# Performance work log

Hardware: AMD Instinct MI355X
Metric: run time of the kernel (lower is better)

## Reference

```python
import jax, jax.numpy as jnp
import numpy as np

K = 3          # kernel size
STRIDE = 1
PAD = 1
GROUPS = 32    # GroupNorm groups
EPS = 1e-5


def setup_inputs() -> dict:
    key = jax.random.key(0)
    ks = jax.random.split(key, 6)
    B, Cin, H, W, Cout = 4, 256, 64, 64, 256
    K2 = K * K
    x = jax.random.normal(ks[0], (B, Cin, H, W), jnp.float32)
    offset = jax.random.normal(ks[1], (B, 2 * K2, H, W), jnp.float32)
    mask = jax.random.uniform(ks[2], (B, K2, H, W), jnp.float32)
    weight = jax.random.normal(ks[3], (Cout, Cin, K, K), jnp.float32) * (1.0 / np.sqrt(Cin * K2))
    bias = jnp.zeros((Cout,), jnp.float32)
    gamma = jnp.ones((Cout,), jnp.float32)   # constant_init(norm, 1)
    beta = jnp.zeros((Cout,), jnp.float32)   # bias=0
    return {"x": x, "offset": offset, "mask": mask, "weight": weight,
            "bias": bias, "gamma": gamma, "beta": beta}


def _modulated_deform_conv(x, offset, mask, weight, bias):
    """DCNv2: bilinear-sample x at learned offsets, modulate by mask, conv-accumulate."""
    B, Cin, H, W = x.shape
    Cout = weight.shape[0]
    K2 = K * K
    Ho = (H + 2 * PAD - K) // STRIDE + 1
    Wo = (W + 2 * PAD - K) // STRIDE + 1

    # base sampling grid per kernel point: [K2, Ho, Wo]
    ky, kx = jnp.meshgrid(jnp.arange(K), jnp.arange(K), indexing='ij')
    ky = ky.reshape(K2).astype(jnp.float32)
    kx = kx.reshape(K2).astype(jnp.float32)
    hs = (jnp.arange(Ho) * STRIDE - PAD).astype(jnp.float32)
    ws = (jnp.arange(Wo) * STRIDE - PAD).astype(jnp.float32)

    off = offset.reshape(B, K2, 2, Ho, Wo)  # interleaved (dy, dx) per kernel point
    y = ky[None, :, None, None] + hs[None, None, :, None] + off[:, :, 0]   # [B,K2,Ho,Wo]
    xc = kx[None, :, None, None] + ws[None, None, None, :] + off[:, :, 1]  # [B,K2,Ho,Wo]

    y0 = jnp.floor(y)
    x0 = jnp.floor(xc)
    dy = y - y0
    dx = xc - x0
    y0i = y0.astype(jnp.int32)
    x0i = x0.astype(jnp.int32)

    x_flat = x.reshape(B, Cin, H * W)

    def corner(yi, xi, w):
        # corner-wise zero padding outside the image (matches mmcv bilinear)
        valid = (yi >= 0) & (yi <= H - 1) & (xi >= 0) & (xi <= W - 1)
        idx = jnp.clip(yi, 0, H - 1) * W + jnp.clip(xi, 0, W - 1)  # [B,K2,Ho,Wo]
        idx_f = idx.reshape(B, -1)
        v = jax.vmap(lambda xf, i: xf[:, i])(x_flat, idx_f)  # [B, Cin, K2*Ho*Wo]
        wv = (w * valid.astype(w.dtype)).reshape(B, 1, -1)
        return v * wv

    val = (corner(y0i,     x0i,     (1 - dy) * (1 - dx))
         + corner(y0i,     x0i + 1, (1 - dy) * dx)
         + corner(y0i + 1, x0i,     dy * (1 - dx))
         + corner(y0i + 1, x0i + 1, dy * dx))
    val = val.reshape(B, Cin, K2, Ho, Wo) * mask[:, None]  # modulate

    w_r = weight.reshape(Cout, Cin, K2)
    out = jnp.einsum('bckhw,ock->bohw', val, w_r) + bias[None, :, None, None]
    return out


def _group_norm(x, gamma, beta):
    B, C, H, W = x.shape
    g = x.reshape(B, GROUPS, C // GROUPS, H, W)
    mu = g.mean(axis=(2, 3, 4), keepdims=True)
    var = ((g - mu) ** 2).mean(axis=(2, 3, 4), keepdims=True)
    g = (g - mu) * jax.lax.rsqrt(var + EPS)
    return g.reshape(B, C, H, W) * gamma[None, :, None, None] + beta[None, :, None, None]


def reference(x, offset, mask, weight, bias, gamma, beta):
    out = _modulated_deform_conv(x, offset, mask, weight, bias)
    out = _group_norm(out, gamma, beta)
    return jax.nn.relu(out)
```

## Files before the change

### kernel.cpp

```cpp
#include <hip/hip_runtime.h>
#include <math.h>

#define BB    4
#define CIN   256
#define HH    64
#define WWID  64
#define COUT  256
#define KKS   3
#define K2    9
#define PADV  1
#define HWSZ  4096
#define GROUPS 32
#define CPG   8
#define EPSV  1e-5f
#define ROWB  4608
#define NKC   36

typedef __attribute__((ext_vector_type(8))) short bf16x8;
typedef __attribute__((ext_vector_type(4))) float f32x4;

#define GLOAD_LDS16(g, l) \
    __builtin_amdgcn_global_load_lds((const __attribute__((address_space(1))) unsigned int*)(g), \
                                     (__attribute__((address_space(3))) unsigned int*)(l), 16, 0, 0)

__device__ __forceinline__ unsigned short f2bf(float f) {
    unsigned u = __float_as_uint(f);
    u = (u + 0x7fffu + ((u >> 16) & 1u)) >> 16;
    return (unsigned short)u;
}
__device__ __forceinline__ float bflo(unsigned q) { return __uint_as_float(q << 16); }
__device__ __forceinline__ float bfhi(unsigned q) { return __uint_as_float(q & 0xffff0000u); }
__device__ __forceinline__ void fma8(float* f, float w, uint4 q) {
    f[0] += w * bflo(q.x); f[1] += w * bfhi(q.x);
    f[2] += w * bflo(q.y); f[3] += w * bfhi(q.y);
    f[4] += w * bflo(q.z); f[5] += w * bfhi(q.z);
    f[6] += w * bflo(q.w); f[7] += w * bfhi(q.w);
}

__global__ __launch_bounds__(256)
void k_pre(const float* __restrict__ x, unsigned short* __restrict__ xh,
           const float* __restrict__ w, unsigned short* __restrict__ wtb,
           float* __restrict__ gstat) {
    int t = threadIdx.x;
    if (blockIdx.x < 128) {
        __shared__ float tile[32][33];
        int hw0 = blockIdx.x * 32;
        int c0  = blockIdx.y * 32;
        int b   = blockIdx.z;
        int tx = t & 31, ty = t >> 5;
        const float* xp = x + (size_t)b * CIN * HWSZ;
        #pragma unroll
        for (int i = 0; i < 4; i++)
            tile[ty + i * 8][tx] = xp[(c0 + ty + i * 8) * HWSZ + hw0 + tx];
        __syncthreads();
        int j = t >> 3, cq = t & 7;
        union { unsigned short s[4]; uint2 d; } pk;
        #pragma unroll
        for (int k = 0; k < 4; k++) pk.s[k] = f2bf(tile[cq * 4 + k][j]);
        *(uint2*)((char*)xh + ((size_t)b * HWSZ * CIN + (size_t)(hw0 + j) * CIN + c0 + cq * 4) * 2) = pk.d;
    } else {
        if (blockIdx.y == 0 && blockIdx.z == 0)
            for (int i = t; i < BB * GROUPS * 2 + 8; i += 256) gstat[i] = 0.f;
        int idx = (blockIdx.y * 4 + blockIdx.z) * 256 + t;
        int co = idx >> 5, c8 = idx & 31;
        int cin0 = c8 * 8;
        int q = c8 >> 3, c = c8 & 7;
        int pc = c ^ (co & 7);
        for (int k2 = 0; k2 < K2; k2++) {
            union { unsigned short s[8]; uint4 qq; } pk;
            #pragma unroll
            for (int j = 0; j < 8; j++)
                pk.s[j] = f2bf(w[(co * CIN + cin0 + j) * K2 + k2]);
            int phys = co * ROWB + k2 * 512 + q * 128 + pc * 16;
            *(uint4*)((char*)wtb + phys) = pk.qq;
        }
    }
}

__global__ __launch_bounds__(256)
void k_conv(const unsigned short* __restrict__ wtb, const unsigned short* __restrict__ xh,
            const float* __restrict__ offset, const float* __restrict__ mask,
            const float* __restrict__ bias, float* __restrict__ out,
            float* __restrict__ gstat) {
    __shared__ unsigned short As[128 * 64];
    __shared__ unsigned short Bs[64 * 64];
    __shared__ int   cidx[64 * K2 * 4];
    __shared__ float cwgt[64 * K2 * 4];
    __shared__ float gs[16], gss[16];

    int lid = blockIdx.x;
    int j8  = lid >> 3;
    int mt  = j8 & 1;
    int strip = (lid & 7) * 32 + (j8 >> 1);
    int b = strip >> 6;
    int hwbase = (strip & 63) * 64;
    int m0 = mt * 128;

    int t = threadIdx.x, w = t >> 6, l = t & 63;
    int r16 = l & 15, half = l >> 4;
    int wm = w & 1, wn = w >> 1;
    int skey = r16 & 7;

    if (t < 16) { gs[t] = 0.f; gss[t] = 0.f; }

    for (int i = t; i < 64 * K2; i += 256) {
        int px = i / K2, k2 = i - px * K2;
        int hw = hwbase + px;
        int ho = hw >> 6, wo = hw & 63;
        int ky = k2 / KKS, kx = k2 - ky * KKS;
        float dy = offset[((b * (2 * K2) + k2 * 2 + 0) * HWSZ) + hw];
        float dx = offset[((b * (2 * K2) + k2 * 2 + 1) * HWSZ) + hw];
        float m  = mask[(b * K2 + k2) * HWSZ + hw];
        float y  = (float)(ky + ho - PADV) + dy;
        float xc = (float)(kx + wo - PADV) + dx;
        float y0f = floorf(y), x0f = floorf(xc);
        float fy = y - y0f, fx = xc - x0f;
        int y0 = (int)y0f, x0 = (int)x0f;
        int   yy[2] = { y0, y0 + 1 };
        int   xx[2] = { x0, x0 + 1 };
        float wy[2] = { 1.f - fy, fy };
        float wx[2] = { 1.f - fx, fx };
        #pragma unroll
        for (int ii = 0; ii < 2; ii++)
            #pragma unroll
            for (int jj = 0; jj < 2; jj++) {
                int yi = yy[ii], xi = xx[jj];
                bool valid = (yi >= 0) && (yi < HH) && (xi >= 0) && (xi < WWID);
                int yc  = min(max(yi, 0), HH - 1);
                int xcc = min(max(xi, 0), WWID - 1);
                cidx[i * 4 + ii * 2 + jj] = yc * WWID + xcc;
                cwgt[i * 4 + ii * 2 + jj] = valid ? (wy[ii] * wx[jj] * m) : 0.f;
            }
    }

    const char* ag[4]; unsigned short* lA[4];
    #pragma unroll
    for (int i = 0; i < 4; i++) {
        int o = i * 256 + t;
        ag[i] = (const char*)wtb + (size_t)(m0 + (o >> 3)) * ROWB + (o & 7) * 16;
        lA[i] = (unsigned short*)As + o * 8;
    }

    int sc  = t & 7;
    int px0 = t >> 3;
    const char* xb = (const char*)xh + (size_t)b * HWSZ * CIN * 2;
    int bofs0 = px0 * 64 + (sc ^ (px0 & 7)) * 8;
    int px1 = px0 + 32;
    int bofs1 = px1 * 64 + (sc ^ (px1 & 7)) * 8;

    f32x4 acc[4][2];
    #pragma unroll
    for (int mi = 0; mi < 4; mi++)
        #pragma unroll
        for (int ni = 0; ni < 2; ni++) acc[mi][ni] = (f32x4)0.f;

    __syncthreads();

    uint4 g[2][4]; float gw[2][4];
    #pragma unroll
    for (int it = 0; it < 2; it++) {
        int cb = ((it ? px1 : px0) * K2) * 4;
        #pragma unroll
        for (int c = 0; c < 4; c++) {
            gw[it][c] = cwgt[cb + c];
            g[it][c]  = *(const uint4*)(xb + (size_t)cidx[cb + c] * 512 + sc * 16);
        }
    }

    for (int kc = 0; kc < NKC; kc++) {
        #pragma unroll
        for (int i = 0; i < 4; i++) { GLOAD_LDS16(ag[i], lA[i]); ag[i] += 128; }

        #pragma unroll
        for (int it = 0; it < 2; it++) {
            float f[8] = {0,0,0,0,0,0,0,0};
            fma8(f, gw[it][0], g[it][0]); fma8(f, gw[it][1], g[it][1]);
            fma8(f, gw[it][2], g[it][2]); fma8(f, gw[it][3], g[it][3]);
            union { unsigned short s[8]; uint4 qq; } pk;
            #pragma unroll
            for (int e = 0; e < 8; e++) pk.s[e] = f2bf(f[e]);
            *(uint4*)&Bs[it ? bofs1 : bofs0] = pk.qq;
        }
        __syncthreads();

        if (kc < NKC - 1) {
            int kn = kc + 1;
            int k2n = kn >> 2, qn = kn & 3;
            #pragma unroll
            for (int it = 0; it < 2; it++) {
                int cb = ((it ? px1 : px0) * K2 + k2n) * 4;
                #pragma unroll
                for (int c = 0; c < 4; c++) {
                    gw[it][c] = cwgt[cb + c];
                    g[it][c]  = *(const uint4*)(xb + (size_t)cidx[cb + c] * 512 + qn * 128 + sc * 16);
                }
            }
        }

        #pragma unroll
        for (int ks = 0; ks < 2; ks++) {
            int up = ((ks * 4 + half) ^ skey) * 8;
            bf16x8 af[4], bv[2];
            #pragma unroll
            for (int mi = 0; mi < 4; mi++)
                af[mi] = *(const bf16x8*)&As[(wm * 64 + mi * 16 + r16) * 64 + up];
            #pragma unroll
            for (int ni = 0; ni < 2; ni++)
                bv[ni] = *(const bf16x8*)&Bs[(wn * 32 + ni * 16 + r16) * 64 + up];
            #pragma unroll
            for (int mi = 0; mi < 4; mi++)
                #pragma unroll
                for (int ni = 0; ni < 2; ni++)
                    acc[mi][ni] = __builtin_amdgcn_mfma_f32_16x16x32_bf16(
                        af[mi], bv[ni], acc[mi][ni], 0, 0, 0);
        }
        __syncthreads();
    }

    float s4[4] = {0,0,0,0}, ss4[4] = {0,0,0,0};
    #pragma unroll
    for (int mi = 0; mi < 4; mi++) {
        #pragma unroll
        for (int r = 0; r < 4; r++) {
            int co = m0 + wm * 64 + mi * 16 + half * 4 + r;
            float bs = bias[co];
            float* orow = out + ((size_t)(b * COUT + co)) * HWSZ;
            #pragma unroll
            for (int ni = 0; ni < 2; ni++) {
                int n = hwbase + wn * 32 + ni * 16 + r16;
                float v = acc[mi][ni][r] + bs;
                orow[n] = v;
                s4[mi] += v; ss4[mi] += v * v;
            }
        }
    }
    int gb = half >> 1;
    #pragma unroll
    for (int mi = 0; mi < 4; mi++) {
        atomicAdd(&gs [wm * 8 + mi * 2 + gb], s4[mi]);
        atomicAdd(&gss[wm * 8 + mi * 2 + gb], ss4[mi]);
    }
    __syncthreads();
    if (t < 16) {
        int gidx = (m0 >> 3) + t;
        atomicAdd(&gstat[(b * GROUPS + gidx) * 2 + 0], gs[t]);
        atomicAdd(&gstat[(b * GROUPS + gidx) * 2 + 1], gss[t]);
    }
}

__global__ __launch_bounds__(256)
void k_gnfinal(float* __restrict__ out, const float* __restrict__ gstat,
               const float* __restrict__ gamma, const float* __restrict__ beta) {
    int i4 = blockIdx.x * 256 + threadIdx.x;
    int e  = i4 * 4;
    int c  = (e >> 12) & 255;
    int b  = e >> 20;
    int g  = c >> 3;
    float s  = gstat[((b * GROUPS) + g) * 2 + 0];
    float ss = gstat[((b * GROUPS) + g) * 2 + 1];
    const float inv = 1.f / (float)(CPG * HWSZ);
    float mu  = s * inv;
    float var = ss * inv - mu * mu;
    float rstd = rsqrtf(var + EPSV);
    float ga = gamma[c] * rstd;
    float be = beta[c] - mu * ga;
    float4 v = ((float4*)out)[i4];
    v.x = fmaxf(v.x * ga + be, 0.f);
    v.y = fmaxf(v.y * ga + be, 0.f);
    v.z = fmaxf(v.z * ga + be, 0.f);
    v.w = fmaxf(v.w * ga + be, 0.f);
    ((float4*)out)[i4] = v;
}

extern "C" void kernel_launch(void* const* d_in, const int* in_sizes, int n_in,
                              void* d_out, int out_size, void* d_ws, size_t ws_size,
                              hipStream_t stream) {
    const float* x      = (const float*)d_in[0];
    const float* offset = (const float*)d_in[1];
    const float* mask   = (const float*)d_in[2];
    const float* weight = (const float*)d_in[3];
    const float* bias   = (const float*)d_in[4];
    const float* gamma  = (const float*)d_in[5];
    const float* beta   = (const float*)d_in[6];
    float* out = (float*)d_out;

    unsigned short* xh    = (unsigned short*)d_ws;
    unsigned short* wtb   = xh + (size_t)4194304;
    float*          gstat = (float*)(wtb + (size_t)589824);

    k_pre<<<dim3(129, 8, 4), 256, 0, stream>>>(x, xh, weight, wtb, gstat);
    k_conv<<<512, 256, 0, stream>>>(wtb, xh, offset, mask, bias, out, gstat);
    k_gnfinal<<<(size_t)BB * COUT * HWSZ / 1024, 256, 0, stream>>>(out, gstat, gamma, beta);
}
```

Measured before the change: 154.0 us.

## Retile deform conv to full-Cout blocks over 32-pixel strips, gather once per pixel

Each block now computes all 256 output channels for a 32-pixel strip instead of 128 channels for 64 pixels. Every bilinear gather and blend of the sampled input is therefore done once per pixel rather than duplicated across two channel-tile blocks. The blend also uses packed float2 FMAs and the v_cvt_pk_bf16_f32 conversion, and stores precomputed byte offsets with vector LDS reads. The cost is a larger A tile in LDS and a smaller N per block, so each block loads twice as much weight data per pixel, which may lower occupancy.

```diff
diff --git a/kernel.cpp b/kernel.cpp
--- a/kernel.cpp
+++ b/kernel.cpp
@@ -18,6 +18,7 @@
 
 typedef __attribute__((ext_vector_type(8))) short bf16x8;
 typedef __attribute__((ext_vector_type(4))) float f32x4;
+typedef __attribute__((ext_vector_type(2))) float f32x2;
 
 #define GLOAD_LDS16(g, l) \
     __builtin_amdgcn_global_load_lds((const __attribute__((address_space(1))) unsigned int*)(g), \
@@ -28,13 +29,16 @@
     u = (u + 0x7fffu + ((u >> 16) & 1u)) >> 16;
     return (unsigned short)u;
 }
-__device__ __forceinline__ float bflo(unsigned q) { return __uint_as_float(q << 16); }
-__device__ __forceinline__ float bfhi(unsigned q) { return __uint_as_float(q & 0xffff0000u); }
-__device__ __forceinline__ void fma8(float* f, float w, uint4 q) {
-    f[0] += w * bflo(q.x); f[1] += w * bfhi(q.x);
-    f[2] += w * bflo(q.y); f[3] += w * bfhi(q.y);
-    f[4] += w * bflo(q.z); f[5] += w * bfhi(q.z);
-    f[6] += w * bflo(q.w); f[7] += w * bfhi(q.w);
+__device__ __forceinline__ f32x2 up2(unsigned q) {
+    f32x2 v;
+    v.x = __uint_as_float(q << 16);
+    v.y = __uint_as_float(q & 0xffff0000u);
+    return v;
+}
+__device__ __forceinline__ unsigned cvtpk(f32x2 f) {
+    unsigned r;
+    asm("v_cvt_pk_bf16_f32 %0, %1, %2" : "=v"(r) : "v"(f.x), "v"(f.y));
+    return r;
 }
 
 __global__ __launch_bounds__(256)
@@ -82,28 +86,24 @@
             const float* __restrict__ offset, const float* __restrict__ mask,
             const float* __restrict__ bias, float* __restrict__ out,
             float* __restrict__ gstat) {
-    __shared__ unsigned short As[128 * 64];
-    __shared__ unsigned short Bs[64 * 64];
-    __shared__ int   cidx[64 * K2 * 4];
-    __shared__ float cwgt[64 * K2 * 4];
-    __shared__ float gs[16], gss[16];
+    __shared__ __align__(16) unsigned short As[256 * 64];
+    __shared__ __align__(16) unsigned short Bs[32 * 64];
+    __shared__ __align__(16) int   cidx[32 * K2 * 4];
+    __shared__ __align__(16) float cwgt[32 * K2 * 4];
+    __shared__ float gs[32], gss[32];
 
     int lid = blockIdx.x;
-    int j8  = lid >> 3;
-    int mt  = j8 & 1;
-    int strip = (lid & 7) * 32 + (j8 >> 1);
-    int b = strip >> 6;
-    int hwbase = (strip & 63) * 64;
-    int m0 = mt * 128;
+    int strip = (lid & 7) * 64 + (lid >> 3);
+    int b = strip >> 7;
+    int hwbase = (strip & 127) * 32;
 
     int t = threadIdx.x, w = t >> 6, l = t & 63;
-    int r16 = l & 15, half = l >> 4;
-    int wm = w & 1, wn = w >> 1;
+    int r16 = l & 15, hf = l >> 4;
     int skey = r16 & 7;
 
-    if (t < 16) { gs[t] = 0.f; gss[t] = 0.f; }
-
-    for (int i = t; i < 64 * K2; i += 256) {
+    if (t < 32) { gs[t] = 0.f; gss[t] = 0.f; }
+
+    for (int i = t; i < 32 * K2; i += 256) {
         int px = i / K2, k2 = i - px * K2;
         int hw = hwbase + px;
         int ho = hw >> 6, wo = hw & 63;
@@ -128,25 +128,18 @@
                 bool valid = (yi >= 0) && (yi < HH) && (xi >= 0) && (xi < WWID);
                 int yc  = min(max(yi, 0), HH - 1);
                 int xcc = min(max(xi, 0), WWID - 1);
-                cidx[i * 4 + ii * 2 + jj] = yc * WWID + xcc;
+                cidx[i * 4 + ii * 2 + jj] = (yc * WWID + xcc) << 9;
                 cwgt[i * 4 + ii * 2 + jj] = valid ? (wy[ii] * wx[jj] * m) : 0.f;
             }
     }
 
-    const char* ag[4]; unsigned short* lA[4];
-    #pragma unroll
-    for (int i = 0; i < 4; i++) {
-        int o = i * 256 + t;
-        ag[i] = (const char*)wtb + (size_t)(m0 + (o >> 3)) * ROWB + (o & 7) * 16;
-        lA[i] = (unsigned short*)As + o * 8;
-    }
+    const char* agb = (const char*)wtb + (size_t)(t >> 3) * ROWB + (t & 7) * 16;
+    unsigned short* lA = (unsigned short*)As + t * 8;
 
     int sc  = t & 7;
     int px0 = t >> 3;
-    const char* xb = (const char*)xh + (size_t)b * HWSZ * CIN * 2;
+    const char* xb = (const char*)xh + (size_t)b * HWSZ * CIN * 2 + sc * 16;
     int bofs0 = px0 * 64 + (sc ^ (px0 & 7)) * 8;
-    int px1 = px0 + 32;
-    int bofs1 = px1 * 64 + (sc ^ (px1 & 7)) * 8;
 
     f32x4 acc[4][2];
     #pragma unroll
@@ -156,57 +149,64 @@
 
     __syncthreads();
 
-    uint4 g[2][4]; float gw[2][4];
-    #pragma unroll
-    for (int it = 0; it < 2; it++) {
-        int cb = ((it ? px1 : px0) * K2) * 4;
-        #pragma unroll
-        for (int c = 0; c < 4; c++) {
-            gw[it][c] = cwgt[cb + c];
-            g[it][c]  = *(const uint4*)(xb + (size_t)cidx[cb + c] * 512 + sc * 16);
-        }
+    uint4 g[4]; float gw[4];
+    {
+        int cb = (px0 * K2) * 4;
+        int4   ci = *(const int4*)&cidx[cb];
+        float4 cw = *(const float4*)&cwgt[cb];
+        gw[0] = cw.x; gw[1] = cw.y; gw[2] = cw.z; gw[3] = cw.w;
+        g[0] = *(const uint4*)(xb + ci.x);
+        g[1] = *(const uint4*)(xb + ci.y);
+        g[2] = *(const uint4*)(xb + ci.z);
+        g[3] = *(const uint4*)(xb + ci.w);
     }
 
     for (int kc = 0; kc < NKC; kc++) {
         #pragma unroll
-        for (int i = 0; i < 4; i++) { GLOAD_LDS16(ag[i], lA[i]); ag[i] += 128; }
-
-        #pragma unroll
-        for (int it = 0; it < 2; it++) {
-            float f[8] = {0,0,0,0,0,0,0,0};
-            fma8(f, gw[it][0], g[it][0]); fma8(f, gw[it][1], g[it][1]);
-            fma8(f, gw[it][2], g[it][2]); fma8(f, gw[it][3], g[it][3]);
-            union { unsigned short s[8]; uint4 qq; } pk;
-            #pragma unroll
-            for (int e = 0; e < 8; e++) pk.s[e] = f2bf(f[e]);
-            *(uint4*)&Bs[it ? bofs1 : bofs0] = pk.qq;
+        for (int i = 0; i < 8; i++)
+            GLOAD_LDS16(agb + (size_t)i * (32 * (size_t)ROWB), lA + i * 2048);
+        agb += 128;
+
+        {
+            f32x2 f0 = {0.f, 0.f}, f1 = {0.f, 0.f}, f2 = {0.f, 0.f}, f3 = {0.f, 0.f};
+            #pragma unroll
+            for (int c = 0; c < 4; c++) {
+                f32x2 wv = { gw[c], gw[c] };
+                f0 = __builtin_elementwise_fma(wv, up2(g[c].x), f0);
+                f1 = __builtin_elementwise_fma(wv, up2(g[c].y), f1);
+                f2 = __builtin_elementwise_fma(wv, up2(g[c].z), f2);
+                f3 = __builtin_elementwise_fma(wv, up2(g[c].w), f3);
+            }
+            uint4 pk;
+            pk.x = cvtpk(f0); pk.y = cvtpk(f1); pk.z = cvtpk(f2); pk.w = cvtpk(f3);
+            *(uint4*)&Bs[bofs0] = pk;
         }
         __syncthreads();
 
         if (kc < NKC - 1) {
             int kn = kc + 1;
             int k2n = kn >> 2, qn = kn & 3;
-            #pragma unroll
-            for (int it = 0; it < 2; it++) {
-                int cb = ((it ? px1 : px0) * K2 + k2n) * 4;
-                #pragma unroll
-                for (int c = 0; c < 4; c++) {
-                    gw[it][c] = cwgt[cb + c];
-                    g[it][c]  = *(const uint4*)(xb + (size_t)cidx[cb + c] * 512 + qn * 128 + sc * 16);
-                }
-            }
+            int cb = (px0 * K2 + k2n) * 4;
+            int4   ci = *(const int4*)&cidx[cb];
+            float4 cw = *(const float4*)&cwgt[cb];
+            gw[0] = cw.x; gw[1] = cw.y; gw[2] = cw.z; gw[3] = cw.w;
+            const char* xq = xb + qn * 128;
+            g[0] = *(const uint4*)(xq + ci.x);
+            g[1] = *(const uint4*)(xq + ci.y);
+            g[2] = *(const uint4*)(xq + ci.z);
+            g[3] = *(const uint4*)(xq + ci.w);
         }
 
         #pragma unroll
         for (int ks = 0; ks < 2; ks++) {
-            int up = ((ks * 4 + half) ^ skey) * 8;
+            int up = ((ks * 4 + hf) ^ skey) * 8;
             bf16x8 af[4], bv[2];
             #pragma unroll
             for (int mi = 0; mi < 4; mi++)
-                af[mi] = *(const bf16x8*)&As[(wm * 64 + mi * 16 + r16) * 64 + up];
+                af[mi] = *(const bf16x8*)&As[(w * 64 + mi * 16 + r16) * 64 + up];
             #pragma unroll
             for (int ni = 0; ni < 2; ni++)
-                bv[ni] = *(const bf16x8*)&Bs[(wn * 32 + ni * 16 + r16) * 64 + up];
+                bv[ni] = *(const bf16x8*)&Bs[(ni * 16 + r16) * 64 + up];
             #pragma unroll
             for (int mi = 0; mi < 4; mi++)
                 #pragma unroll
@@ -222,29 +222,28 @@
     for (int mi = 0; mi < 4; mi++) {
         #pragma unroll
         for (int r = 0; r < 4; r++) {
-            int co = m0 + wm * 64 + mi * 16 + half * 4 + r;
+            int co = w * 64 + mi * 16 + hf * 4 + r;
             float bs = bias[co];
             float* orow = out + ((size_t)(b * COUT + co)) * HWSZ;
             #pragma unroll
             for (int ni = 0; ni < 2; ni++) {
-                int n = hwbase + wn * 32 + ni * 16 + r16;
+                int n = hwbase + ni * 16 + r16;
                 float v = acc[mi][ni][r] + bs;
                 orow[n] = v;
                 s4[mi] += v; ss4[mi] += v * v;
             }
         }
     }
-    int gb = half >> 1;
+    int gb = hf >> 1;
     #pragma unroll
     for (int mi = 0; mi < 4; mi++) {
-        atomicAdd(&gs [wm * 8 + mi * 2 + gb], s4[mi]);
-        atomicAdd(&gss[wm * 8 + mi * 2 + gb], ss4[mi]);
+        atomicAdd(&gs [w * 8 + mi * 2 + gb], s4[mi]);
+        atomicAdd(&gss[w * 8 + mi * 2 + gb], ss4[mi]);
     }
     __syncthreads();
-    if (t < 16) {
-        int gidx = (m0 >> 3) + t;
-        atomicAdd(&gstat[(b * GROUPS + gidx) * 2 + 0], gs[t]);
-        atomicAdd(&gstat[(b * GROUPS + gidx) * 2 + 1], gss[t]);
+    if (t < 32) {
+        atomicAdd(&gstat[(b * GROUPS + t) * 2 + 0], gs[t]);
+        atomicAdd(&gstat[(b * GROUPS + t) * 2 + 1], gss[t]);
     }
 }
 
```

Measured after the change: 154.4 us. About the same (+0.3%).
